# Optimization experiments

Hardware: AMD Instinct MI355X
Metric: run time of the kernel (lower is better)

Reference implementation:

```python
import jax, jax.numpy as jnp
import numpy as np


def _make_kernels():
    # 4 fixed 3x3x3 stencils: identity + Sobel x/y/z (separable smooth x smooth x derivative)
    d = np.array([-1.0, 0.0, 1.0], dtype=np.float32)
    s = np.array([1.0, 2.0, 1.0], dtype=np.float32)
    sx = np.einsum('i,j,k->ijk', s, s, d) / 16.0
    sy = np.einsum('i,j,k->ijk', s, d, s) / 16.0
    sz = np.einsum('i,j,k->ijk', d, s, s) / 16.0
    ident = np.zeros((3, 3, 3), dtype=np.float32)
    ident[1, 1, 1] = 1.0
    return np.stack([ident, sx, sy, sz], axis=0)  # (4,3,3,3)


def setup_inputs() -> dict:
    key = jax.random.key(0)
    x = jax.random.normal(key, (4, 16, 64, 64, 64), dtype=jnp.float32)
    kernels = jnp.asarray(_make_kernels())  # fixed buffer, (4,3,3,3)
    return {"x": x, "kernels": kernels}


def reference(x, kernels):
    B, C, D, H, W = x.shape
    # replicate padding by 1 on each spatial side
    xp = jnp.pad(x, ((0, 0), (0, 0), (1, 1), (1, 1), (1, 1)), mode='edge')
    # depthwise: every channel gets all 4 filters -> fold channels into batch,
    # run one conv with 4 output channels, then restore torch's [k*C + c] ordering
    xr = xp.reshape(B * C, 1, D + 2, H + 2, W + 2)
    k = kernels[:, None]  # (4,1,3,3,3), OIDHW
    out = jax.lax.conv_general_dilated(
        xr, k, window_strides=(1, 1, 1), padding='VALID',
        dimension_numbers=('NCDHW', 'OIDHW', 'NCDHW'))  # (B*C,4,D,H,W)
    out = out.reshape(B, C, 4, D, H, W).transpose(0, 2, 1, 3, 4, 5)
    return out.reshape(B, 4 * C, D, H, W)
```

## Files before the change

kernel.cpp:

```cpp
#include <hip/hip_runtime.h>


#define B_ 4
#define C_ 16
#define D_ 64
#define H_ 64
#define W_ 64

__global__ __launch_bounds__(256) void perceive3d_kernel(
    const float* __restrict__ x, float* __restrict__ out)
{
    const int w  = threadIdx.x;
    const int h  = blockIdx.x * blockDim.y + threadIdx.y;
    const int d  = blockIdx.y;
    const int bc = blockIdx.z;
    const int b  = bc >> 4;
    const int c  = bc & 15;

    const int wm = (w == 0)      ? 0        : w - 1;
    const int wp = (w == W_ - 1) ? (W_ - 1) : w + 1;

    const float* xb = x + (size_t)bc * (D_ * H_ * W_);

    float sW[3][3];
    float dW[3][3];
    float center = 0.0f;

#pragma unroll
    for (int i = 0; i < 3; ++i) {
        int dz = d + i - 1;
        dz = (dz < 0) ? 0 : ((dz > D_ - 1) ? D_ - 1 : dz);
#pragma unroll
        for (int j = 0; j < 3; ++j) {
            int hy = h + j - 1;
            hy = (hy < 0) ? 0 : ((hy > H_ - 1) ? H_ - 1 : hy);
            const float* row = xb + ((size_t)dz * H_ + hy) * W_;
            float am = row[wm];
            float ac = row[w];
            float ap = row[wp];
            sW[i][j] = am + 2.0f * ac + ap;
            dW[i][j] = ap - am;
            if (i == 1 && j == 1) center = ac;
        }
    }

    const float sx = ( (dW[0][0] + 2.0f * dW[0][1] + dW[0][2])
            + 2.0f * (dW[1][0] + 2.0f * dW[1][1] + dW[1][2])
            +        (dW[2][0] + 2.0f * dW[2][1] + dW[2][2]) ) * (1.0f / 16.0f);

    const float sy = (        (sW[0][2] - sW[0][0])
                     + 2.0f * (sW[1][2] - sW[1][0])
                     +        (sW[2][2] - sW[2][0]) ) * (1.0f / 16.0f);

    const float sz = (        (sW[2][0] - sW[0][0])
                     + 2.0f * (sW[2][1] - sW[0][1])
                     +        (sW[2][2] - sW[0][2]) ) * (1.0f / 16.0f);

    const size_t dhw     = (size_t)D_ * H_ * W_;
    const size_t spatial = ((size_t)d * H_ + h) * W_ + w;
    const size_t cdhw    = (size_t)C_ * dhw;

    float* o = out + ((size_t)(b * 4) * C_ + c) * dhw + spatial;
    o[0 * cdhw] = center;
    o[1 * cdhw] = sx;
    o[2 * cdhw] = sy;
    o[3 * cdhw] = sz;
}

extern "C" void kernel_launch(void* const* d_in, const int* in_sizes, int n_in,
                              void* d_out, int out_size, void* d_ws, size_t ws_size,
                              hipStream_t stream) {
    (void)in_sizes; (void)n_in; (void)d_ws; (void)ws_size; (void)out_size;
    const float* x = (const float*)d_in[0];
    float* out = (float*)d_out;

    dim3 block(W_, 4, 1);
    dim3 grid(H_ / 4, D_, B_ * C_);
    perceive3d_kernel<<<grid, block, 0, stream>>>(x, out);
}
```

Measured before the change: 371.0 us.

## Vectorize stencil to float4 per thread with lane shuffles and nontemporal stores

Each thread now loads and computes four consecutive W outputs using float4 loads. It gets the W-neighbour values through wavefront shuffles instead of separate scalar loads. The Sobel sums are accumulated directly into vector registers, and the four outputs are written with nontemporal float4 stores. This cuts the number of memory instructions and redundant neighbour loads and aims to keep the large output stream from polluting the cache. The cost is fewer threads per block-row, so less parallelism per output element.

```diff
diff --git a/kernel.cpp b/kernel.cpp
--- a/kernel.cpp
+++ b/kernel.cpp
@@ -7,64 +7,75 @@
 #define H_ 64
 #define W_ 64
 
+typedef float float4v __attribute__((ext_vector_type(4)));
+
 __global__ __launch_bounds__(256) void perceive3d_kernel(
     const float* __restrict__ x, float* __restrict__ out)
 {
-    const int w  = threadIdx.x;
-    const int h  = blockIdx.x * blockDim.y + threadIdx.y;
-    const int d  = blockIdx.y;
-    const int bc = blockIdx.z;
-    const int b  = bc >> 4;
-    const int c  = bc & 15;
-
-    const int wm = (w == 0)      ? 0        : w - 1;
-    const int wp = (w == W_ - 1) ? (W_ - 1) : w + 1;
+    const int lane = threadIdx.x;
+    const int quad = lane & 15;
+    const int hsub = lane >> 4;
+    const int h    = blockIdx.x * 16 + threadIdx.y * 4 + hsub;
+    const int d    = blockIdx.y;
+    const int bc   = blockIdx.z;
+    const int b    = bc >> 4;
+    const int c    = bc & 15;
 
     const float* xb = x + (size_t)bc * (D_ * H_ * W_);
 
-    float sW[3][3];
-    float dW[3][3];
-    float center = 0.0f;
+    const int dm = (d == 0) ? 0 : d - 1;
+    const int dp = (d == D_ - 1) ? D_ - 1 : d + 1;
+    const int hm = (h == 0) ? 0 : h - 1;
+    const int hp = (h == H_ - 1) ? H_ - 1 : h + 1;
+
+    const int dzo[3] = { dm * (H_ * W_), d * (H_ * W_), dp * (H_ * W_) };
+    const int hyo[3] = { hm * W_,        h * W_,        hp * W_ };
+    const float si[3] = { 1.0f, 2.0f, 1.0f };
+
+    float4v sx = {0,0,0,0}, sy = {0,0,0,0}, sz = {0,0,0,0};
+    float4v center = {0,0,0,0};
 
 #pragma unroll
     for (int i = 0; i < 3; ++i) {
-        int dz = d + i - 1;
-        dz = (dz < 0) ? 0 : ((dz > D_ - 1) ? D_ - 1 : dz);
 #pragma unroll
         for (int j = 0; j < 3; ++j) {
-            int hy = h + j - 1;
-            hy = (hy < 0) ? 0 : ((hy > H_ - 1) ? H_ - 1 : hy);
-            const float* row = xb + ((size_t)dz * H_ + hy) * W_;
-            float am = row[wm];
-            float ac = row[w];
-            float ap = row[wp];
-            sW[i][j] = am + 2.0f * ac + ap;
-            dW[i][j] = ap - am;
-            if (i == 1 && j == 1) center = ac;
+            const float* row = xb + dzo[i] + hyo[j];
+            float4v q = *(const float4v*)(row + 4 * quad);
+
+            float left  = __shfl_up(q.w, 1);
+            float right = __shfl_down(q.x, 1);
+            if (quad == 0)      left  = q.x;
+            if (quad == 15)     right = q.w;
+
+            float4v am = { left, q.x, q.y, q.z };
+            float4v ap = { q.y, q.z, q.w, right };
+
+            float4v sw = am + 2.0f * q + ap;
+            float4v dw = ap - am;
+
+            const float cij = si[i] * si[j];
+            sx += cij * dw;
+            if (j == 0)      sy -= si[i] * sw;
+            else if (j == 2) sy += si[i] * sw;
+            if (i == 0)      sz -= si[j] * sw;
+            else if (i == 2) sz += si[j] * sw;
+            if (i == 1 && j == 1) center = q;
         }
     }
 
-    const float sx = ( (dW[0][0] + 2.0f * dW[0][1] + dW[0][2])
-            + 2.0f * (dW[1][0] + 2.0f * dW[1][1] + dW[1][2])
-            +        (dW[2][0] + 2.0f * dW[2][1] + dW[2][2]) ) * (1.0f / 16.0f);
-
-    const float sy = (        (sW[0][2] - sW[0][0])
-                     + 2.0f * (sW[1][2] - sW[1][0])
-                     +        (sW[2][2] - sW[2][0]) ) * (1.0f / 16.0f);
-
-    const float sz = (        (sW[2][0] - sW[0][0])
-                     + 2.0f * (sW[2][1] - sW[0][1])
-                     +        (sW[2][2] - sW[0][2]) ) * (1.0f / 16.0f);
+    sx *= (1.0f / 16.0f);
+    sy *= (1.0f / 16.0f);
+    sz *= (1.0f / 16.0f);
 
     const size_t dhw     = (size_t)D_ * H_ * W_;
-    const size_t spatial = ((size_t)d * H_ + h) * W_ + w;
     const size_t cdhw    = (size_t)C_ * dhw;
+    const size_t spatial = ((size_t)d * H_ + h) * W_ + 4 * quad;
 
     float* o = out + ((size_t)(b * 4) * C_ + c) * dhw + spatial;
-    o[0 * cdhw] = center;
-    o[1 * cdhw] = sx;
-    o[2 * cdhw] = sy;
-    o[3 * cdhw] = sz;
+    __builtin_nontemporal_store(center, (float4v*)(o + 0 * cdhw));
+    __builtin_nontemporal_store(sx,     (float4v*)(o + 1 * cdhw));
+    __builtin_nontemporal_store(sy,     (float4v*)(o + 2 * cdhw));
+    __builtin_nontemporal_store(sz,     (float4v*)(o + 3 * cdhw));
 }
 
 extern "C" void kernel_launch(void* const* d_in, const int* in_sizes, int n_in,
@@ -74,7 +85,7 @@
     const float* x = (const float*)d_in[0];
     float* out = (float*)d_out;
 
-    dim3 block(W_, 4, 1);
-    dim3 grid(H_ / 4, D_, B_ * C_);
+    dim3 block(64, 4, 1);
+    dim3 grid(H_ / 16, D_, B_ * C_);
     perceive3d_kernel<<<grid, block, 0, stream>>>(x, out);
 }
```

After: 315.3 us. 1.18x faster.
